# Kernel optimization log

Hardware: AMD Instinct MI355X
Metric: run time of the kernel (lower is better)

## Reference

```python
import jax, jax.numpy as jnp
import numpy as np

GRID_SIDE = 32          # grid_side
H = 512                 # hidden dim
SEQ = 8192              # sequence length
DX = 1.0                # grid spacing (fixed in __init__)


def setup_inputs() -> dict:
    key = jax.random.key(0)
    ks = jax.random.split(key, 8)
    G = GRID_SIDE * GRID_SIDE
    x = jax.random.normal(ks[0], (SEQ, H), dtype=jnp.float32)
    c = jax.random.normal(ks[1], (G,), dtype=jnp.float32) * 0.1
    kp_diag = jax.random.normal(ks[2], (GRID_SIDE,), dtype=jnp.float32) * 0.1
    k_diag = jax.random.normal(ks[3], (GRID_SIDE,), dtype=jnp.float32) * 0.1
    dt_matrix = jax.random.normal(ks[4], (GRID_SIDE, GRID_SIDE), dtype=jnp.float32) * 0.1
    B = jax.random.normal(ks[5], (G, H), dtype=jnp.float32) * 0.01
    C = jax.random.normal(ks[6], (H, G), dtype=jnp.float32) * 0.01
    D = jax.random.uniform(ks[7], (H,), dtype=jnp.float32) * 0.01
    return dict(x=x, c=c, kp_diag=kp_diag, k_diag=k_diag,
                dt_matrix=dt_matrix, B=B, C=C, D=D)


def _fdtd_forward(x, c, kp_diag, k_diag, dt_matrix, B, C, D):
    gs = GRID_SIDE
    G = gs * gs
    dx = DX
    sp = jax.nn.softplus

    # ---- get_positive_parameters ----
    c_pos = sp(c)
    kp_d = jnp.clip(sp(kp_diag), 1e-4, 0.2)
    k_d = jnp.clip(sp(k_diag), 1e-4, 0.2)
    dt2d = jnp.clip(jnp.exp(dt_matrix), 0.1, 5.0)           # [gs, gs]
    max_c = 0.7 * dx / dt2d
    c_pos = jnp.clip(c_pos.reshape(gs, gs), 0.01, 0.9 * max_c).reshape(-1)
    dt = dt2d.reshape(-1)                                    # [G]

    # ---- input projection ----
    Bu = x @ B.T                                             # [S, G]

    # ---- apply_fdtd: extra softplus+clip on diag params (as in source) ----
    kp_d2 = jnp.clip(sp(kp_d), 1e-4, 0.5)
    k_d2 = jnp.clip(sp(k_d), 1e-4, 0.5)

    # ---- construct_fdtd_eigendecomposition ----
    idx = jnp.arange(0, G, gs + 1)[:gs]
    kp_full = jnp.zeros((G,), dtype=x.dtype).at[idx].set(kp_d2)
    k_full = jnp.zeros((G,), dtype=x.dtype).at[idx].set(k_d2)
    kp_full = jnp.clip(sp(kp_full), 1e-4, 0.5)
    k_full = jnp.clip(sp(k_full), 1e-4, 0.5)
    xi = jnp.pi / (2 * dx)
    dt_s = jnp.clip(dt, 0.1, 5.0)
    d1 = jnp.maximum(1.0 + dt_s * k_full, 0.1)
    d2 = jnp.maximum(1.0 + dt_s * kp_full, 0.1)
    lam1 = 1.0 / d1
    real_part = 0.5 * (1.0 / d2 + 1.0 / d1)
    c_safe = jnp.clip(c_pos, 0.01, 1.0)
    imag_part = jnp.clip(c_safe * dt_s * xi / jnp.sqrt(jnp.maximum(d1 * d2, 1e-6)), -10.0, 10.0)
    lam2 = (real_part + 1j * imag_part).astype(jnp.complex64)
    lam3 = (real_part - 1j * imag_part).astype(jnp.complex64)
    factor = (1j * imag_part / jnp.maximum(jnp.abs(real_part - lam1), 1e-3)).astype(jnp.complex64)

    # ---- modal forcing ----
    scaling = 1.0 / (1.0 + dt * kp_full)                     # [G]
    sBu = (Bu * scaling).astype(jnp.complex64)               # [S, G]
    zeros = jnp.zeros_like(sBu)
    F = jnp.concatenate([zeros, sBu, jnp.conjugate(sBu)], axis=1)        # [S, 3G]
    Lambda = jnp.concatenate([lam1.astype(jnp.complex64), lam2, lam3])   # [3G]
    lam_seq = jnp.broadcast_to(Lambda, F.shape)

    # ---- diagonal linear recurrence via associative scan ----
    def binop(left, right):
        A1, b1 = left
        A2, b2 = right
        return (A2 * A1, A2 * b1 + b2)

    _, b_all = jax.lax.associative_scan(binop, (lam_seq, F))  # [S, 3G]

    m1 = b_all[:, :G]
    m2 = b_all[:, G:2 * G]
    m3 = b_all[:, 2 * G:]
    p = jnp.real(m2 + m3)                                     # pressure field [S, G]
    # ox = oy = real(m1 + factor*m2 + conj(factor)*m3) (unused in output)

    # ---- output projection + skip (y = C p + D x) ----
    out = p @ C.T + x * D                                     # [S, H]
    return out


def reference(x, c, kp_diag, k_diag, dt_matrix, B, C, D):
    return _fdtd_forward(x, c, kp_diag, k_diag, dt_matrix, B, C, D)
```

## Files before the change

### kernel.cpp

```cpp
#include <hip/hip_runtime.h>
#include <math.h>


#define SEQ 8192
#define HDIM 512
#define GS 32
#define G 1024
#define CHUNK 128
#define NCH (SEQ / CHUNK)

typedef unsigned short u16;
typedef unsigned int u32;
typedef __attribute__((ext_vector_type(8))) short short8;
typedef __attribute__((ext_vector_type(4))) float f32x4;

#define AS1 __attribute__((address_space(1)))
#define AS3 __attribute__((address_space(3)))

__device__ __forceinline__ float softplusf(float z) {
    return fmaxf(z, 0.0f) + log1pf(expf(-fabsf(z)));
}
__device__ __forceinline__ float clipf(float v, float lo, float hi) {
    return fminf(fmaxf(v, lo), hi);
}
__device__ __forceinline__ void split2(float f, u16& h, u16& l) {
    u32 b = __float_as_uint(f);
    u32 hb = (b + 0x8000u) & 0xffff0000u;
    h = (u16)(hb >> 16);
    float r = f - __uint_as_float(hb);
    l = (u16)((__float_as_uint(r) + 0x8000u) >> 16);
}

__global__ void params_kernel(const float* __restrict__ c,
                              const float* __restrict__ kp_diag,
                              const float* __restrict__ k_diag,
                              const float* __restrict__ dt_matrix,
                              float* __restrict__ lam_re, float* __restrict__ lam_im,
                              float* __restrict__ scal,
                              float* __restrict__ lamC_re, float* __restrict__ lamC_im) {
    int g = blockIdx.x * blockDim.x + threadIdx.x;
    if (g >= G) return;
    float dt = clipf(expf(dt_matrix[g]), 0.1f, 5.0f);
    float max_c = 0.7f / dt;
    float c_pos = clipf(softplusf(c[g]), 0.01f, 0.9f * max_c);

    float kp_base = 0.0f, k_base = 0.0f;
    if (g % (GS + 1) == 0) {
        int d = g / (GS + 1);
        float kp_d = clipf(softplusf(kp_diag[d]), 1e-4f, 0.2f);
        kp_base = clipf(softplusf(kp_d), 1e-4f, 0.5f);
        float k_d = clipf(softplusf(k_diag[d]), 1e-4f, 0.2f);
        k_base = clipf(softplusf(k_d), 1e-4f, 0.5f);
    }
    float kp_full = clipf(softplusf(kp_base), 1e-4f, 0.5f);
    float k_full  = clipf(softplusf(k_base),  1e-4f, 0.5f);

    float d1 = fmaxf(1.0f + dt * k_full, 0.1f);
    float d2 = fmaxf(1.0f + dt * kp_full, 0.1f);
    float real_part = 0.5f * (1.0f / d2 + 1.0f / d1);
    float c_safe = clipf(c_pos, 0.01f, 1.0f);
    const float xi = 1.5707963267948966f;
    float imag_part = clipf(c_safe * dt * xi / sqrtf(fmaxf(d1 * d2, 1e-6f)), -10.0f, 10.0f);

    lam_re[g] = real_part;
    lam_im[g] = imag_part;
    scal[g] = 1.0f / (1.0f + dt * kp_full);

    float ar = real_part, ai = imag_part;
#pragma unroll
    for (int s = 0; s < 7; ++s) {
        float nr = ar * ar - ai * ai;
        float ni = 2.0f * ar * ai;
        ar = nr; ai = ni;
    }
    lamC_re[g] = ar; lamC_im[g] = ai;
}

__global__ __launch_bounds__(256)
void split_bf16(const float* __restrict__ in, u16* __restrict__ hi,
                u16* __restrict__ lo, int n4) {
    int stride = gridDim.x * 256;
    for (int i = blockIdx.x * 256 + threadIdx.x; i < n4; i += stride) {
        float4 v = ((const float4*)in)[i];
        ushort4 h, l;
        split2(v.x, h.x, l.x); split2(v.y, h.y, l.y);
        split2(v.z, h.z, l.z); split2(v.w, h.w, l.w);
        ((ushort4*)hi)[i] = h;
        ((ushort4*)lo)[i] = l;
    }
}

template<int BM, int BN, int WM, int WN, bool SCALE_EPI>
__global__ __launch_bounds__(256, 2)
void gemm_split(const u16* __restrict__ Ah, const u16* __restrict__ Al,
                const u16* __restrict__ Bh, const u16* __restrict__ Bl,
                float* __restrict__ Cout, int M, int N, int K,
                const float* __restrict__ scal,
                const float* __restrict__ xres, const float* __restrict__ Dv) {
    constexpr int MI = WM / 16, NI = WN / 16;
    constexpr int ACH = BM / 16, BCH = BN / 16;
    constexpr int oAh = 0, oAl = BM * 32;
    constexpr int oBh = 2 * BM * 32, oBl = 2 * BM * 32 + BN * 32;
    constexpr int BUFS = 2 * BM * 32 + 2 * BN * 32;
    __shared__ __align__(16) u16 sm[2][BUFS];

    const int tid = threadIdx.x;
    const int lane = tid & 63, wid = tid >> 6;
    const int wrow = wid >> 1, wcol = wid & 1;
    const int lr = lane & 15, lg = lane >> 4;

    const int flat = blockIdx.y * gridDim.x + blockIdx.x;
    const int cpx = (gridDim.x * gridDim.y) >> 3;
    const int swz = (flat & 7) * cpx + (flat >> 3);
    const int m0 = (swz / gridDim.x) * BM, n0 = (swz % gridDim.x) * BN;

    const u16* gbs[4]   = {Ah, Al, Bh, Bl};
    const int  nchs[4]  = {ACH, ACH, BCH, BCH};
    const int  row0s[4] = {m0, m0, n0, n0};
    const int  ofss[4]  = {oAh, oAl, oBh, oBl};

    const int srow = lane >> 2;
    const int shp  = lane & 3;

    auto stage = [&](int buf, int kt) {
#pragma unroll
        for (int a = 0; a < 4; ++a) {
            for (int c = wid; c < nchs[a]; c += 4) {
                int r = c * 16 + srow;
                int h = shp ^ ((r >> 1) & 3);
                const u16* gp = gbs[a] + (size_t)(row0s[a] + r) * K + kt + h * 8;
                u16* lp = &sm[buf][ofss[a] + c * 512];
                __builtin_amdgcn_global_load_lds((const AS1 u32*)gp, (AS3 u32*)lp, 16, 0, 0);
            }
        }
    };

    f32x4 acc[MI][NI];
#pragma unroll
    for (int i = 0; i < MI; ++i)
#pragma unroll
        for (int j = 0; j < NI; ++j) acc[i][j] = (f32x4){0.f, 0.f, 0.f, 0.f};

    stage(0, 0);
    __syncthreads();

    const int NT = K / 32;
    for (int t = 0; t < NT; ++t) {
        const int buf = t & 1;
        if (t + 1 < NT) stage(buf ^ 1, (t + 1) * 32);

        short8 fah[MI], fal[MI], fbh[NI], fbl[NI];
#pragma unroll
        for (int mi = 0; mi < MI; ++mi) {
            int r = wrow * WM + mi * 16 + lr;
            int idx = r * 32 + ((lg ^ ((r >> 1) & 3)) * 8);
            fah[mi] = *(const short8*)&sm[buf][oAh + idx];
            fal[mi] = *(const short8*)&sm[buf][oAl + idx];
        }
#pragma unroll
        for (int ni = 0; ni < NI; ++ni) {
            int r = wcol * WN + ni * 16 + lr;
            int idx = r * 32 + ((lg ^ ((r >> 1) & 3)) * 8);
            fbh[ni] = *(const short8*)&sm[buf][oBh + idx];
            fbl[ni] = *(const short8*)&sm[buf][oBl + idx];
        }
#pragma unroll
        for (int mi = 0; mi < MI; ++mi)
#pragma unroll
            for (int ni = 0; ni < NI; ++ni) {
                acc[mi][ni] = __builtin_amdgcn_mfma_f32_16x16x32_bf16(fah[mi], fbh[ni], acc[mi][ni], 0, 0, 0);
                acc[mi][ni] = __builtin_amdgcn_mfma_f32_16x16x32_bf16(fah[mi], fbl[ni], acc[mi][ni], 0, 0, 0);
                acc[mi][ni] = __builtin_amdgcn_mfma_f32_16x16x32_bf16(fal[mi], fbh[ni], acc[mi][ni], 0, 0, 0);
            }
        __syncthreads();
    }

#pragma unroll
    for (int mi = 0; mi < MI; ++mi)
#pragma unroll
        for (int ni = 0; ni < NI; ++ni) {
            int col = n0 + wcol * WN + ni * 16 + lr;
            int rbase = m0 + wrow * WM + mi * 16 + lg * 4;
            if constexpr (SCALE_EPI) {
                float s = scal[col];
#pragma unroll
                for (int v = 0; v < 4; ++v)
                    Cout[(size_t)(rbase + v) * N + col] = acc[mi][ni][v] * s;
            } else {
                float dv = Dv[col];
#pragma unroll
                for (int v = 0; v < 4; ++v) {
                    size_t o = (size_t)(rbase + v) * N + col;
                    Cout[o] = fmaf(xres[o], dv, acc[mi][ni][v]);
                }
            }
        }
}

__global__ __launch_bounds__(256)
void scan_carry(const float* __restrict__ sBu,
                const float* __restrict__ lam_re, const float* __restrict__ lam_im,
                float2* __restrict__ carry) {
    int g = blockIdx.x * 256 + threadIdx.x;
    int ch = blockIdx.y;
    const float lr = lam_re[g], li = lam_im[g];
    const float* f = sBu + (size_t)ch * CHUNK * G + g;
    float hr = 0.0f, hi = 0.0f;
    for (int tb = 0; tb < CHUNK / 8; ++tb) {
        float fb[8];
#pragma unroll
        for (int u = 0; u < 8; ++u) fb[u] = f[(size_t)(tb * 8 + u) * G];
#pragma unroll
        for (int u = 0; u < 8; ++u) {
            float nr = fmaf(lr, hr, fmaf(-li, hi, fb[u]));
            float ni = fmaf(lr, hi, li * hr);
            hr = nr; hi = ni;
        }
    }
    carry[(size_t)ch * G + g] = make_float2(hr, hi);
}

__global__ void carry_scan(const float2* __restrict__ carry,
                           const float* __restrict__ lamC_re, const float* __restrict__ lamC_im,
                           float2* __restrict__ carry_in) {
    int g = blockIdx.x * blockDim.x + threadIdx.x;
    if (g >= G) return;
    const float lr = lamC_re[g], li = lamC_im[g];
    float hr = 0.0f, hi = 0.0f;
    for (int cb = 0; cb < NCH; cb += 8) {
        float2 loc[8];
#pragma unroll
        for (int u = 0; u < 8; ++u) loc[u] = carry[(size_t)(cb + u) * G + g];
#pragma unroll
        for (int u = 0; u < 8; ++u) {
            carry_in[(size_t)(cb + u) * G + g] = make_float2(hr, hi);
            float nr = fmaf(lr, hr, -li * hi) + loc[u].x;
            float ni = fmaf(lr, hi, li * hr) + loc[u].y;
            hr = nr; hi = ni;
        }
    }
}

__global__ __launch_bounds__(256)
void scan_emit(const float* __restrict__ sBu, u16* __restrict__ ph, u16* __restrict__ pl,
               const float* __restrict__ lam_re, const float* __restrict__ lam_im,
               const float2* __restrict__ carry_in) {
    int g = blockIdx.x * 256 + threadIdx.x;
    int ch = blockIdx.y;
    const float lr = lam_re[g], li = lam_im[g];
    const float* f = sBu + (size_t)ch * CHUNK * G + g;
    u16* oh = ph + (size_t)ch * CHUNK * G + g;
    u16* ol = pl + (size_t)ch * CHUNK * G + g;
    float2 h0 = carry_in[(size_t)ch * G + g];
    float hr = h0.x, hi = h0.y;
    for (int tb = 0; tb < CHUNK / 8; ++tb) {
        float fb[8];
#pragma unroll
        for (int u = 0; u < 8; ++u) fb[u] = f[(size_t)(tb * 8 + u) * G];
#pragma unroll
        for (int u = 0; u < 8; ++u) {
            float nr = fmaf(lr, hr, fmaf(-li, hi, fb[u]));
            float ni = fmaf(lr, hi, li * hr);
            hr = nr; hi = ni;
            float p = 2.0f * hr;
            u16 hh, ll; split2(p, hh, ll);
            oh[(size_t)(tb * 8 + u) * G] = hh;
            ol[(size_t)(tb * 8 + u) * G] = ll;
        }
    }
}

extern "C" void kernel_launch(void* const* d_in, const int* in_sizes, int n_in,
                              void* d_out, int out_size, void* d_ws, size_t ws_size,
                              hipStream_t stream) {
    const float* x   = (const float*)d_in[0];
    const float* c   = (const float*)d_in[1];
    const float* kp  = (const float*)d_in[2];
    const float* kd  = (const float*)d_in[3];
    const float* dtm = (const float*)d_in[4];
    const float* B   = (const float*)d_in[5];
    const float* Cm  = (const float*)d_in[6];
    const float* D   = (const float*)d_in[7];
    float* out = (float*)d_out;

    char* w = (char*)d_ws;
    float* sBu = (float*)w;              w += (size_t)SEQ * G * 4;
    u16* ph = (u16*)w;                   w += (size_t)SEQ * G * 2;
    u16* pl = (u16*)w;                   w += (size_t)SEQ * G * 2;
    u16* xh = (u16*)w;                   w += (size_t)SEQ * HDIM * 2;
    u16* xl = (u16*)w;                   w += (size_t)SEQ * HDIM * 2;
    u16* Bh_ = (u16*)w;                  w += (size_t)G * HDIM * 2;
    u16* Bl_ = (u16*)w;                  w += (size_t)G * HDIM * 2;
    u16* Ch_ = (u16*)w;                  w += (size_t)HDIM * G * 2;
    u16* Cl_ = (u16*)w;                  w += (size_t)HDIM * G * 2;
    float* lam_re  = (float*)w;          w += G * 4;
    float* lam_im  = (float*)w;          w += G * 4;
    float* scal    = (float*)w;          w += G * 4;
    float* lamC_re = (float*)w;          w += G * 4;
    float* lamC_im = (float*)w;          w += G * 4;
    float2* carry    = (float2*)w;       w += (size_t)NCH * G * 8;
    float2* carry_in = (float2*)w;

    params_kernel<<<dim3(G / 256), 256, 0, stream>>>(c, kp, kd, dtm, lam_re, lam_im,
                                                     scal, lamC_re, lamC_im);
    split_bf16<<<dim3(2048), 256, 0, stream>>>(x,  xh,  xl,  SEQ * HDIM / 4);
    split_bf16<<<dim3(512),  256, 0, stream>>>(B,  Bh_, Bl_, G * HDIM / 4);
    split_bf16<<<dim3(512),  256, 0, stream>>>(Cm, Ch_, Cl_, HDIM * G / 4);

    gemm_split<128, 128, 64, 64, true>
        <<<dim3(G / 128, SEQ / 128), 256, 0, stream>>>(xh, xl, Bh_, Bl_, sBu,
                                                       SEQ, G, HDIM, scal, nullptr, nullptr);

    scan_carry<<<dim3(G / 256, NCH), 256, 0, stream>>>(sBu, lam_re, lam_im, carry);
    carry_scan<<<dim3(G / 256), 256, 0, stream>>>(carry, lamC_re, lamC_im, carry_in);
    scan_emit<<<dim3(G / 256, NCH), 256, 0, stream>>>(sBu, ph, pl, lam_re, lam_im, carry_in);

    gemm_split<128, 64, 64, 32, false>
        <<<dim3(HDIM / 64, SEQ / 128), 256, 0, stream>>>(ph, pl, Ch_, Cl_, out,
                                                         SEQ, HDIM, G, nullptr, x, D);
}
```

Measured before the change: 184.4 us.

## Triple-buffer GEMM LDS pipeline with vmcnt waits and merge split kernels

The split-bf16 GEMM now keeps three LDS stages in flight, prefetching two K-tiles ahead. Full __syncthreads are replaced by explicit s_waitcnt vmcnt counts plus raw s_barrier, so global-to-LDS loads overlap with MFMA work instead of draining every iteration. The three bf16 split launches are also merged into one kernel to cut launch overhead. In exchange, LDS per block grows by half, which may reduce occupancy at two blocks per CU, and the hand-counted vmcnt values must match the number of loads each wave issues.

```diff
diff --git a/kernel.cpp b/kernel.cpp
--- a/kernel.cpp
+++ b/kernel.cpp
@@ -29,6 +29,13 @@
     h = (u16)(hb >> 16);
     float r = f - __uint_as_float(hb);
     l = (u16)((__float_as_uint(r) + 0x8000u) >> 16);
+}
+template<int N> __device__ __forceinline__ void waitv() {
+    if constexpr (N == 0)       asm volatile("s_waitcnt vmcnt(0)" ::: "memory");
+    else if constexpr (N == 6)  asm volatile("s_waitcnt vmcnt(6)" ::: "memory");
+    else if constexpr (N == 8)  asm volatile("s_waitcnt vmcnt(8)" ::: "memory");
+    else if constexpr (N == 12) asm volatile("s_waitcnt vmcnt(12)" ::: "memory");
+    else if constexpr (N == 16) asm volatile("s_waitcnt vmcnt(16)" ::: "memory");
 }
 
 __global__ void params_kernel(const float* __restrict__ c,
@@ -76,17 +83,25 @@
     lamC_re[g] = ar; lamC_im[g] = ai;
 }
 
+#define N4X (SEQ * HDIM / 4)
+#define N4B (G * HDIM / 4)
+#define N4C (HDIM * G / 4)
 __global__ __launch_bounds__(256)
-void split_bf16(const float* __restrict__ in, u16* __restrict__ hi,
-                u16* __restrict__ lo, int n4) {
+void split_all(const float* __restrict__ x,  u16* __restrict__ xh,  u16* __restrict__ xl,
+               const float* __restrict__ B,  u16* __restrict__ Bh,  u16* __restrict__ Bl,
+               const float* __restrict__ Cm, u16* __restrict__ Ch,  u16* __restrict__ Cl) {
     int stride = gridDim.x * 256;
-    for (int i = blockIdx.x * 256 + threadIdx.x; i < n4; i += stride) {
-        float4 v = ((const float4*)in)[i];
+    for (int i = blockIdx.x * 256 + threadIdx.x; i < N4X + N4B + N4C; i += stride) {
+        const float* in; u16* hi; u16* lo; int j = i;
+        if (j < N4X) { in = x; hi = xh; lo = xl; }
+        else if (j < N4X + N4B) { j -= N4X; in = B; hi = Bh; lo = Bl; }
+        else { j -= N4X + N4B; in = Cm; hi = Ch; lo = Cl; }
+        float4 v = ((const float4*)in)[j];
         ushort4 h, l;
         split2(v.x, h.x, l.x); split2(v.y, h.y, l.y);
         split2(v.z, h.z, l.z); split2(v.w, h.w, l.w);
-        ((ushort4*)hi)[i] = h;
-        ((ushort4*)lo)[i] = l;
+        ((ushort4*)hi)[j] = h;
+        ((ushort4*)lo)[j] = l;
     }
 }
 
@@ -102,7 +117,8 @@
     constexpr int oAh = 0, oAl = BM * 32;
     constexpr int oBh = 2 * BM * 32, oBl = 2 * BM * 32 + BN * 32;
     constexpr int BUFS = 2 * BM * 32 + 2 * BN * 32;
-    __shared__ __align__(16) u16 sm[2][BUFS];
+    constexpr int LPW = (ACH + BCH) / 2;
+    __shared__ __align__(16) u16 sm[3][BUFS];
 
     const int tid = threadIdx.x;
     const int lane = tid & 63, wid = tid >> 6;
@@ -141,28 +157,38 @@
 #pragma unroll
         for (int j = 0; j < NI; ++j) acc[i][j] = (f32x4){0.f, 0.f, 0.f, 0.f};
 
+    const int NT = K / 32;
     stage(0, 0);
-    __syncthreads();
-
-    const int NT = K / 32;
+    stage(1, 32);
+    int cur = 0;
     for (int t = 0; t < NT; ++t) {
-        const int buf = t & 1;
-        if (t + 1 < NT) stage(buf ^ 1, (t + 1) * 32);
-
+        if (t + 2 < NT) {
+            int nb = cur + 2; if (nb >= 3) nb -= 3;
+            stage(nb, (t + 2) * 32);
+        }
+        const int rem = NT - 1 - t;
+        if (rem >= 2)      waitv<2 * LPW>();
+        else if (rem == 1) waitv<LPW>();
+        else               waitv<0>();
+        __builtin_amdgcn_sched_barrier(0);
+        __builtin_amdgcn_s_barrier();
+        __builtin_amdgcn_sched_barrier(0);
+
+        const u16* smc = sm[cur];
         short8 fah[MI], fal[MI], fbh[NI], fbl[NI];
 #pragma unroll
         for (int mi = 0; mi < MI; ++mi) {
             int r = wrow * WM + mi * 16 + lr;
             int idx = r * 32 + ((lg ^ ((r >> 1) & 3)) * 8);
-            fah[mi] = *(const short8*)&sm[buf][oAh + idx];
-            fal[mi] = *(const short8*)&sm[buf][oAl + idx];
+            fah[mi] = *(const short8*)&smc[oAh + idx];
+            fal[mi] = *(const short8*)&smc[oAl + idx];
         }
 #pragma unroll
         for (int ni = 0; ni < NI; ++ni) {
             int r = wcol * WN + ni * 16 + lr;
             int idx = r * 32 + ((lg ^ ((r >> 1) & 3)) * 8);
-            fbh[ni] = *(const short8*)&sm[buf][oBh + idx];
-            fbl[ni] = *(const short8*)&sm[buf][oBl + idx];
+            fbh[ni] = *(const short8*)&smc[oBh + idx];
+            fbl[ni] = *(const short8*)&smc[oBl + idx];
         }
 #pragma unroll
         for (int mi = 0; mi < MI; ++mi)
@@ -172,7 +198,8 @@
                 acc[mi][ni] = __builtin_amdgcn_mfma_f32_16x16x32_bf16(fah[mi], fbl[ni], acc[mi][ni], 0, 0, 0);
                 acc[mi][ni] = __builtin_amdgcn_mfma_f32_16x16x32_bf16(fal[mi], fbh[ni], acc[mi][ni], 0, 0, 0);
             }
-        __syncthreads();
+        __builtin_amdgcn_s_barrier();
+        cur = cur + 1 == 3 ? 0 : cur + 1;
     }
 
 #pragma unroll
@@ -303,9 +330,7 @@
 
     params_kernel<<<dim3(G / 256), 256, 0, stream>>>(c, kp, kd, dtm, lam_re, lam_im,
                                                      scal, lamC_re, lamC_im);
-    split_bf16<<<dim3(2048), 256, 0, stream>>>(x,  xh,  xl,  SEQ * HDIM / 4);
-    split_bf16<<<dim3(512),  256, 0, stream>>>(B,  Bh_, Bl_, G * HDIM / 4);
-    split_bf16<<<dim3(512),  256, 0, stream>>>(Cm, Ch_, Cl_, HDIM * G / 4);
+    split_all<<<dim3(2048), 256, 0, stream>>>(x, xh, xl, B, Bh_, Bl_, Cm, Ch_, Cl_);
 
     gemm_split<128, 128, 64, 64, true>
         <<<dim3(G / 128, SEQ / 128), 256, 0, stream>>>(xh, xl, Bh_, Bl_, sBu,
```

Result: slower. 191.3 us (+3.7%).
